# Kernel tuning notes

Measured on AMD Instinct MI355X. Metric: run time of the kernel, lower is better.

Reference implementation:

```python
import jax, jax.numpy as jnp
import numpy as np

def setup_inputs() -> dict:
    key = jax.random.key(0)
    k1, k2, k3, k4, k5 = jax.random.split(key, 5)
    H = 1024
    B, T = 32, 1024
    hidden = jax.random.normal(k1, (1, B, H), dtype=jnp.float32)
    encoder_outputs = jax.random.normal(k2, (B, T, H), dtype=jnp.float32)
    # nn.Linear(2H, H): weight [H, 2H], bias [H]
    bound = 1.0 / np.sqrt(2 * H)
    W = jax.random.uniform(k3, (H, 2 * H), minval=-bound, maxval=bound, dtype=jnp.float32)
    b = jax.random.uniform(k4, (H,), minval=-bound, maxval=bound, dtype=jnp.float32)
    v = jax.random.uniform(k5, (H,), dtype=jnp.float32)  # torch.rand
    return {"hidden": hidden, "encoder_outputs": encoder_outputs, "W": W, "b": b, "v": v}

def reference(hidden, encoder_outputs, W, b, v):
    B = hidden.shape[1]
    H = hidden.shape[2]
    h = jnp.transpose(hidden, (1, 0, 2)).reshape(B, -1)  # [B, H]
    # Split Linear(2H->H): cat([h_rep, enc]) @ W.T == h @ Wh.T + enc @ We.T
    Wh, We = W[:, :H], W[:, H:]
    # [B,1,H] + [B,T,H] -> [B,T,H]
    pre = jnp.tanh((h @ Wh.T + b)[:, None, :] + jnp.einsum('bth,gh->btg', encoder_outputs, We))
    energies = jnp.einsum('bth,h->bt', pre, v)  # [B, T]
    return jax.nn.softmax(energies, axis=1)[:, None, :]  # [B, 1, T]
```

## Files before the change

kernel.cpp:

```cpp
#include <hip/hip_runtime.h>
#include <hip/hip_fp16.h>

typedef _Float16 half8   __attribute__((ext_vector_type(8)));
typedef _Float16 half4_t __attribute__((ext_vector_type(4)));
typedef float    f32x4   __attribute__((ext_vector_type(4)));

#define HDIM  1024
#define BATCH 32
#define TLEN  1024
#define M_TOT (BATCH * TLEN)

#define BM 128
#define BN 128
#define BKF 64
#define LDA 40

__global__ void prep_k(const float* __restrict__ W, const float* __restrict__ hidden,
                       const float* __restrict__ bias, _Float16* __restrict__ We16,
                       float* __restrict__ q, float* __restrict__ energ) {
    const int bid = blockIdx.x;
    const int t = threadIdx.x;
    if (bid < 1024) {
        int idx = bid * 256 + t;
        int g  = idx >> 8;
        int k4 = idx & 255;
        float4 f = *reinterpret_cast<const float4*>(W + (size_t)g * 2048 + 1024 + k4 * 4);
        half4_t h;
        h[0] = (_Float16)f.x; h[1] = (_Float16)f.y; h[2] = (_Float16)f.z; h[3] = (_Float16)f.w;
        *reinterpret_cast<half4_t*>(We16 + (size_t)idx * 4) = h;
    } else if (bid < 2048) {
        int g = bid - 1024;
        int wave = t >> 6, lane = t & 63;
        float acc[BATCH];
#pragma unroll
        for (int b = 0; b < BATCH; b++) acc[b] = 0.f;
        const float* wr = W + (size_t)g * 2048;
        for (int h = t; h < HDIM; h += 256) {
            float w = wr[h];
#pragma unroll
            for (int b = 0; b < BATCH; b++) acc[b] = fmaf(w, hidden[b * HDIM + h], acc[b]);
        }
        __shared__ float sm[4 * BATCH];
#pragma unroll
        for (int b = 0; b < BATCH; b++) {
            float s = acc[b];
#pragma unroll
            for (int off = 32; off >= 1; off >>= 1) s += __shfl_xor(s, off);
            if (lane == 0) sm[wave * BATCH + b] = s;
        }
        __syncthreads();
        if (t < BATCH) {
            float s = sm[t] + sm[BATCH + t] + sm[2 * BATCH + t] + sm[3 * BATCH + t];
            q[t * HDIM + g] = s + bias[g];
        }
    } else {
        energ[(bid - 2048) * 256 + t] = 0.f;
    }
}

__global__ void enc_convert_k(const float* __restrict__ enc, _Float16* __restrict__ enc16) {
    size_t i = ((size_t)blockIdx.x * blockDim.x + threadIdx.x) * 8;
    float4 f0 = *reinterpret_cast<const float4*>(enc + i);
    float4 f1 = *reinterpret_cast<const float4*>(enc + i + 4);
    half8 h;
    h[0] = (_Float16)f0.x; h[1] = (_Float16)f0.y; h[2] = (_Float16)f0.z; h[3] = (_Float16)f0.w;
    h[4] = (_Float16)f1.x; h[5] = (_Float16)f1.y; h[6] = (_Float16)f1.z; h[7] = (_Float16)f1.w;
    *reinterpret_cast<half8*>(enc16 + i) = h;
}

__device__ __forceinline__ void async16(const void* g, void* l) {
    __builtin_amdgcn_global_load_lds(
        (const __attribute__((address_space(1))) void*)g,
        (__attribute__((address_space(3))) void*)l, 16, 0, 0);
}

__global__ __launch_bounds__(256)
void attn_gemm_lds_k(const _Float16* __restrict__ enc16,
                     const _Float16* __restrict__ We16,
                     const float* __restrict__ q, const float* __restrict__ v,
                     float* __restrict__ energies) {
    __shared__ _Float16 As[BM * BKF];
    __shared__ _Float16 Bs[BN * BKF];

    const int tid  = threadIdx.x;
    const int id   = blockIdx.x;
    const int xcd  = id & 7;
    const int w    = id >> 3;
    const int m0   = (xcd * 32 + (w >> 3)) * BM;
    const int n0   = (w & 7) * BN;
    const int wave = tid >> 6;
    const int lane = tid & 63;
    const int quad = lane >> 4;
    const int l16  = lane & 15;
    const int wm   = (wave & 1) * 64;
    const int wn   = (wave >> 1) * 64;

    f32x4 acc[4][4];
#pragma unroll
    for (int i = 0; i < 4; i++)
#pragma unroll
        for (int j = 0; j < 4; j++) acc[i][j] = {0.f, 0.f, 0.f, 0.f};

    const int srow = wave * 32 + (lane >> 3);
    const int scol = ((lane & 7) ^ (lane >> 3)) * 8;
    const _Float16* gA = enc16 + (size_t)(m0 + srow) * HDIM + scol;
    const _Float16* gB = We16  + (size_t)(n0 + srow) * HDIM + scol;
    _Float16* lA = As + wave * 2048;
    _Float16* lB = Bs + wave * 2048;
    const size_t istep = (size_t)8 * HDIM;

#pragma unroll
    for (int ii = 0; ii < 4; ii++) {
        async16(gA + ii * istep, lA + ii * 512);
        async16(gB + ii * istep, lB + ii * 512);
    }
    __syncthreads();

    int aoff[2][4], boff[2][4];
#pragma unroll
    for (int s = 0; s < 2; s++)
#pragma unroll
        for (int i = 0; i < 4; i++) {
            int ra = wm + i * 16 + l16;
            int rb = wn + i * 16 + l16;
            aoff[s][i] = ra * BKF + (((s * 4 + quad) ^ (l16 & 7)) * 8);
            boff[s][i] = rb * BKF + (((s * 4 + quad) ^ (l16 & 7)) * 8);
        }

    for (int k0 = 0; k0 < HDIM; k0 += BKF) {
        half8 af[2][4], bf[2][4];
#pragma unroll
        for (int s = 0; s < 2; s++)
#pragma unroll
            for (int i = 0; i < 4; i++) {
                af[s][i] = *reinterpret_cast<const half8*>(&As[aoff[s][i]]);
                bf[s][i] = *reinterpret_cast<const half8*>(&Bs[boff[s][i]]);
            }
        __syncthreads();

        if (k0 + BKF < HDIM) {
            const int kn = k0 + BKF;
#pragma unroll
            for (int ii = 0; ii < 4; ii++) {
                async16(gA + kn + ii * istep, lA + ii * 512);
                async16(gB + kn + ii * istep, lB + ii * 512);
            }
        }

#pragma unroll
        for (int s = 0; s < 2; s++)
#pragma unroll
            for (int mi = 0; mi < 4; mi++)
#pragma unroll
                for (int ni = 0; ni < 4; ni++)
                    acc[mi][ni] = __builtin_amdgcn_mfma_f32_16x16x32_f16(af[s][mi], bf[s][ni], acc[mi][ni], 0, 0, 0);

        __syncthreads();
    }

    const int bidx = m0 >> 10;
    float qv[4], vv[4];
#pragma unroll
    for (int ni = 0; ni < 4; ni++) {
        int g = n0 + wn + ni * 16 + l16;
        qv[ni] = q[bidx * HDIM + g];
        vv[ni] = v[g];
    }
#pragma unroll
    for (int mi = 0; mi < 4; mi++) {
#pragma unroll
        for (int r = 0; r < 4; r++) {
            int row = wm + mi * 16 + quad * 4 + r;
            float s = 0.f;
#pragma unroll
            for (int ni = 0; ni < 4; ni++) {
                float pre = acc[mi][ni][r] + qv[ni];
                float e = __expf(2.f * pre);
                float th = 1.f - 2.f / (e + 1.f);
                s = fmaf(th, vv[ni], s);
            }
            s += __shfl_xor(s, 1);
            s += __shfl_xor(s, 2);
            s += __shfl_xor(s, 4);
            s += __shfl_xor(s, 8);
            if (l16 == 0) atomicAdd(&energies[m0 + row], s);
        }
    }
}

__global__ __launch_bounds__(256, 2)
void attn_gemm_k(const float* __restrict__ enc, const _Float16* __restrict__ We16,
                 const float* __restrict__ q, const float* __restrict__ v,
                 float* __restrict__ energies) {
    __shared__ _Float16 As[BM * LDA];
    __shared__ _Float16 Bs[BN * LDA];

    const int tid  = threadIdx.x;
    const int m0   = blockIdx.x * BM;
    const int n0   = blockIdx.y * BN;
    const int wave = tid >> 6;
    const int lane = tid & 63;
    const int quad = lane >> 4;
    const int l16  = lane & 15;
    const int wm   = (wave & 1) * 64;
    const int wn   = (wave >> 1) * 64;

    const int srow = tid >> 1;
    const int scol = (tid & 1) * 16;

    f32x4 acc[4][4];
#pragma unroll
    for (int i = 0; i < 4; i++)
#pragma unroll
        for (int j = 0; j < 4; j++) acc[i][j] = {0.f, 0.f, 0.f, 0.f};

    const float*    ag = enc  + (size_t)(m0 + srow) * HDIM + scol;
    const _Float16* bg = We16 + (size_t)(n0 + srow) * HDIM + scol;
    _Float16* aw = &As[srow * LDA + scol];
    _Float16* bw = &Bs[srow * LDA + scol];

    for (int k0 = 0; k0 < HDIM; k0 += 32) {
        float4 a0 = *reinterpret_cast<const float4*>(ag + k0 + 0);
        float4 a1 = *reinterpret_cast<const float4*>(ag + k0 + 4);
        float4 a2 = *reinterpret_cast<const float4*>(ag + k0 + 8);
        float4 a3 = *reinterpret_cast<const float4*>(ag + k0 + 12);
        float4 b0 = *reinterpret_cast<const float4*>(bg + k0);
        float4 b1 = *reinterpret_cast<const float4*>(bg + k0 + 8);

        __syncthreads();

        half8 ha0, ha1;
        ha0[0] = (_Float16)a0.x; ha0[1] = (_Float16)a0.y; ha0[2] = (_Float16)a0.z; ha0[3] = (_Float16)a0.w;
        ha0[4] = (_Float16)a1.x; ha0[5] = (_Float16)a1.y; ha0[6] = (_Float16)a1.z; ha0[7] = (_Float16)a1.w;
        ha1[0] = (_Float16)a2.x; ha1[1] = (_Float16)a2.y; ha1[2] = (_Float16)a2.z; ha1[3] = (_Float16)a2.w;
        ha1[4] = (_Float16)a3.x; ha1[5] = (_Float16)a3.y; ha1[6] = (_Float16)a3.z; ha1[7] = (_Float16)a3.w;
        *reinterpret_cast<half8*>(aw)     = ha0;
        *reinterpret_cast<half8*>(aw + 8) = ha1;
        *reinterpret_cast<float4*>(bw)     = b0;
        *reinterpret_cast<float4*>(bw + 8) = b1;

        __syncthreads();

        half8 af[4], bf[4];
#pragma unroll
        for (int i = 0; i < 4; i++) {
            af[i] = *reinterpret_cast<const half8*>(&As[(wm + i * 16 + l16) * LDA + quad * 8]);
            bf[i] = *reinterpret_cast<const half8*>(&Bs[(wn + i * 16 + l16) * LDA + quad * 8]);
        }
#pragma unroll
        for (int mi = 0; mi < 4; mi++)
#pragma unroll
            for (int ni = 0; ni < 4; ni++)
                acc[mi][ni] = __builtin_amdgcn_mfma_f32_16x16x32_f16(af[mi], bf[ni], acc[mi][ni], 0, 0, 0);
    }

    const int bidx = m0 >> 10;
    float qv[4], vv[4];
#pragma unroll
    for (int ni = 0; ni < 4; ni++) {
        int g = n0 + wn + ni * 16 + l16;
        qv[ni] = q[bidx * HDIM + g];
        vv[ni] = v[g];
    }
#pragma unroll
    for (int mi = 0; mi < 4; mi++) {
#pragma unroll
        for (int r = 0; r < 4; r++) {
            int row = wm + mi * 16 + quad * 4 + r;
            float s = 0.f;
#pragma unroll
            for (int ni = 0; ni < 4; ni++) {
                float pre = acc[mi][ni][r] + qv[ni];
                float e = __expf(2.f * pre);
                float th = 1.f - 2.f / (e + 1.f);
                s = fmaf(th, vv[ni], s);
            }
            s += __shfl_xor(s, 1);
            s += __shfl_xor(s, 2);
            s += __shfl_xor(s, 4);
            s += __shfl_xor(s, 8);
            if (l16 == 0) atomicAdd(&energies[m0 + row], s);
        }
    }
}

__global__ void softmax_k(const float* __restrict__ energies, float* __restrict__ out) {
    int b = blockIdx.x;
    int t = threadIdx.x;
    int wave = t >> 6, lane = t & 63;
    __shared__ float smax[4], ssum[4];
    float e[4];
#pragma unroll
    for (int i = 0; i < 4; i++) e[i] = energies[b * TLEN + t + i * 256];
    float m = fmaxf(fmaxf(e[0], e[1]), fmaxf(e[2], e[3]));
#pragma unroll
    for (int off = 32; off >= 1; off >>= 1) m = fmaxf(m, __shfl_xor(m, off));
    if (lane == 0) smax[wave] = m;
    __syncthreads();
    float M = fmaxf(fmaxf(smax[0], smax[1]), fmaxf(smax[2], smax[3]));
    float x[4]; float s = 0.f;
#pragma unroll
    for (int i = 0; i < 4; i++) { x[i] = __expf(e[i] - M); s += x[i]; }
#pragma unroll
    for (int off = 32; off >= 1; off >>= 1) s += __shfl_xor(s, off);
    if (lane == 0) ssum[wave] = s;
    __syncthreads();
    float S = ssum[0] + ssum[1] + ssum[2] + ssum[3];
    float inv = 1.f / S;
#pragma unroll
    for (int i = 0; i < 4; i++) out[b * TLEN + t + i * 256] = x[i] * inv;
}

extern "C" void kernel_launch(void* const* d_in, const int* in_sizes, int n_in,
                              void* d_out, int out_size, void* d_ws, size_t ws_size,
                              hipStream_t stream) {
    const float* hidden = (const float*)d_in[0];
    const float* enc    = (const float*)d_in[1];
    const float* W      = (const float*)d_in[2];
    const float* bias   = (const float*)d_in[3];
    const float* v      = (const float*)d_in[4];
    float* out = (float*)d_out;

    char* ws = (char*)d_ws;
    float*    q     = (float*)ws;
    float*    energ = (float*)(ws + 131072);
    _Float16* We16  = (_Float16*)(ws + 262144);
    _Float16* enc16 = (_Float16*)(ws + 262144 + 2097152);
    const size_t need_fast = 262144 + 2097152 + (size_t)M_TOT * HDIM * 2;

    prep_k<<<dim3(2176), 256, 0, stream>>>(W, hidden, bias, We16, q, energ);
    if (ws_size >= need_fast) {
        enc_convert_k<<<dim3((size_t)M_TOT * HDIM / 8 / 256), 256, 0, stream>>>(enc, enc16);
        attn_gemm_lds_k<<<dim3(2048), 256, 0, stream>>>(enc16, We16, q, v, energ);
    } else {
        attn_gemm_k<<<dim3(256, 8), 256, 0, stream>>>(enc, We16, q, v, energ);
    }
    softmax_k<<<dim3(BATCH), 256, 0, stream>>>(energ, out);
}
```

Measured before the change: 317.6 us.

## Double-buffer LDS tiles with smaller K-step to overlap loads and MFMA

```diff
diff --git a/kernel.cpp b/kernel.cpp
--- a/kernel.cpp
+++ b/kernel.cpp
@@ -12,7 +12,7 @@
 
 #define BM 128
 #define BN 128
-#define BKF 64
+#define BKF 32
 #define LDA 40
 
 __global__ void prep_k(const float* __restrict__ W, const float* __restrict__ hidden,
@@ -74,13 +74,13 @@
         (__attribute__((address_space(3))) void*)l, 16, 0, 0);
 }
 
-__global__ __launch_bounds__(256)
+__global__ __launch_bounds__(256, 4)
 void attn_gemm_lds_k(const _Float16* __restrict__ enc16,
                      const _Float16* __restrict__ We16,
                      const float* __restrict__ q, const float* __restrict__ v,
                      float* __restrict__ energies) {
-    __shared__ _Float16 As[BM * BKF];
-    __shared__ _Float16 Bs[BN * BKF];
+    __shared__ _Float16 As[2][BM * BKF];
+    __shared__ _Float16 Bs[2][BN * BKF];
 
     const int tid  = threadIdx.x;
     const int id   = blockIdx.x;
@@ -101,59 +101,49 @@
 #pragma unroll
         for (int j = 0; j < 4; j++) acc[i][j] = {0.f, 0.f, 0.f, 0.f};
 
-    const int srow = wave * 32 + (lane >> 3);
-    const int scol = ((lane & 7) ^ (lane >> 3)) * 8;
-    const _Float16* gA = enc16 + (size_t)(m0 + srow) * HDIM + scol;
-    const _Float16* gB = We16  + (size_t)(n0 + srow) * HDIM + scol;
-    _Float16* lA = As + wave * 2048;
-    _Float16* lB = Bs + wave * 2048;
-    const size_t istep = (size_t)8 * HDIM;
-
-#pragma unroll
-    for (int ii = 0; ii < 4; ii++) {
-        async16(gA + ii * istep, lA + ii * 512);
-        async16(gB + ii * istep, lB + ii * 512);
-    }
+    const int srow   = wave * 32 + (lane >> 2);
+    const int fchunk = (lane & 3) ^ ((lane >> 3) & 3);
+    const _Float16* gA = enc16 + (size_t)(m0 + srow) * HDIM + fchunk * 8;
+    const _Float16* gB = We16  + (size_t)(n0 + srow) * HDIM + fchunk * 8;
+    const size_t istep = (size_t)16 * HDIM;
+    const int ldst = wave * 1024;
+
+    async16(gA, &As[0][ldst]);
+    async16(gA + istep, &As[0][ldst + 512]);
+    async16(gB, &Bs[0][ldst]);
+    async16(gB + istep, &Bs[0][ldst + 512]);
     __syncthreads();
 
-    int aoff[2][4], boff[2][4];
-#pragma unroll
-    for (int s = 0; s < 2; s++)
+    int aoff[4], boff[4];
+#pragma unroll
+    for (int i = 0; i < 4; i++) {
+        int ra = wm + i * 16 + l16;
+        int rb = wn + i * 16 + l16;
+        aoff[i] = ra * BKF + ((quad ^ ((ra >> 1) & 3)) * 8);
+        boff[i] = rb * BKF + ((quad ^ ((rb >> 1) & 3)) * 8);
+    }
+
+    for (int it = 0; it < HDIM / BKF; it++) {
+        const int p = it & 1;
+        if (it + 1 < HDIM / BKF) {
+            const int kn = (it + 1) * BKF;
+            async16(gA + kn, &As[1 - p][ldst]);
+            async16(gA + kn + istep, &As[1 - p][ldst + 512]);
+            async16(gB + kn, &Bs[1 - p][ldst]);
+            async16(gB + kn + istep, &Bs[1 - p][ldst + 512]);
+        }
+
+        half8 af[4], bf[4];
 #pragma unroll
         for (int i = 0; i < 4; i++) {
-            int ra = wm + i * 16 + l16;
-            int rb = wn + i * 16 + l16;
-            aoff[s][i] = ra * BKF + (((s * 4 + quad) ^ (l16 & 7)) * 8);
-            boff[s][i] = rb * BKF + (((s * 4 + quad) ^ (l16 & 7)) * 8);
-        }
-
-    for (int k0 = 0; k0 < HDIM; k0 += BKF) {
-        half8 af[2][4], bf[2][4];
-#pragma unroll
-        for (int s = 0; s < 2; s++)
-#pragma unroll
-            for (int i = 0; i < 4; i++) {
-                af[s][i] = *reinterpret_cast<const half8*>(&As[aoff[s][i]]);
-                bf[s][i] = *reinterpret_cast<const half8*>(&Bs[boff[s][i]]);
-            }
-        __syncthreads();
-
-        if (k0 + BKF < HDIM) {
-            const int kn = k0 + BKF;
-#pragma unroll
-            for (int ii = 0; ii < 4; ii++) {
-                async16(gA + kn + ii * istep, lA + ii * 512);
-                async16(gB + kn + ii * istep, lB + ii * 512);
-            }
-        }
-
-#pragma unroll
-        for (int s = 0; s < 2; s++)
-#pragma unroll
-            for (int mi = 0; mi < 4; mi++)
-#pragma unroll
-                for (int ni = 0; ni < 4; ni++)
-                    acc[mi][ni] = __builtin_amdgcn_mfma_f32_16x16x32_f16(af[s][mi], bf[s][ni], acc[mi][ni], 0, 0, 0);
+            af[i] = *reinterpret_cast<const half8*>(&As[p][aoff[i]]);
+            bf[i] = *reinterpret_cast<const half8*>(&Bs[p][boff[i]]);
+        }
+#pragma unroll
+        for (int mi = 0; mi < 4; mi++)
+#pragma unroll
+            for (int ni = 0; ni < 4; ni++)
+                acc[mi][ni] = __builtin_amdgcn_mfma_f32_16x16x32_f16(af[mi], bf[ni], acc[mi][ni], 0, 0, 0);
 
         __syncthreads();
     }
```

Result: slower. 327.0 us (+3.0%).

## Use 256x256 tiles with register-staged double-buffered LDS in fp16 GEMM

Applied to the files above, without the earlier changes.

```diff
diff --git a/kernel.cpp b/kernel.cpp
--- a/kernel.cpp
+++ b/kernel.cpp
@@ -10,9 +10,10 @@
 #define TLEN  1024
 #define M_TOT (BATCH * TLEN)
 
-#define BM 128
-#define BN 128
-#define BKF 64
+#define BMF 256
+#define BNF 256
+#define BKF 32
+#define NIT (HDIM / BKF)
 #define LDA 40
 
 __global__ void prep_k(const float* __restrict__ W, const float* __restrict__ hidden,
@@ -68,112 +69,137 @@
     *reinterpret_cast<half8*>(enc16 + i) = h;
 }
 
-__device__ __forceinline__ void async16(const void* g, void* l) {
-    __builtin_amdgcn_global_load_lds(
-        (const __attribute__((address_space(1))) void*)g,
-        (__attribute__((address_space(3))) void*)l, 16, 0, 0);
-}
-
-__global__ __launch_bounds__(256)
-void attn_gemm_lds_k(const _Float16* __restrict__ enc16,
+__global__ __launch_bounds__(256, 1)
+void attn_gemm_big_k(const _Float16* __restrict__ enc16,
                      const _Float16* __restrict__ We16,
                      const float* __restrict__ q, const float* __restrict__ v,
                      float* __restrict__ energies) {
-    __shared__ _Float16 As[BM * BKF];
-    __shared__ _Float16 Bs[BN * BKF];
+    __shared__ _Float16 As[2][BMF * BKF];
+    __shared__ _Float16 Bs[2][BNF * BKF];
 
     const int tid  = threadIdx.x;
     const int id   = blockIdx.x;
     const int xcd  = id & 7;
     const int w    = id >> 3;
-    const int m0   = (xcd * 32 + (w >> 3)) * BM;
-    const int n0   = (w & 7) * BN;
+    const int m0   = (xcd * 16 + (w >> 2)) * BMF;
+    const int n0   = (w & 3) * BNF;
     const int wave = tid >> 6;
     const int lane = tid & 63;
     const int quad = lane >> 4;
     const int l16  = lane & 15;
-    const int wm   = (wave & 1) * 64;
-    const int wn   = (wave >> 1) * 64;
-
-    f32x4 acc[4][4];
-#pragma unroll
-    for (int i = 0; i < 4; i++)
-#pragma unroll
-        for (int j = 0; j < 4; j++) acc[i][j] = {0.f, 0.f, 0.f, 0.f};
-
-    const int srow = wave * 32 + (lane >> 3);
-    const int scol = ((lane & 7) ^ (lane >> 3)) * 8;
-    const _Float16* gA = enc16 + (size_t)(m0 + srow) * HDIM + scol;
-    const _Float16* gB = We16  + (size_t)(n0 + srow) * HDIM + scol;
-    _Float16* lA = As + wave * 2048;
-    _Float16* lB = Bs + wave * 2048;
-    const size_t istep = (size_t)8 * HDIM;
-
-#pragma unroll
-    for (int ii = 0; ii < 4; ii++) {
-        async16(gA + ii * istep, lA + ii * 512);
-        async16(gB + ii * istep, lB + ii * 512);
+    const int wm   = (wave & 1) * 128;
+    const int wn   = (wave >> 1) * 128;
+
+    f32x4 acc[8][8];
+#pragma unroll
+    for (int i = 0; i < 8; i++)
+#pragma unroll
+        for (int j = 0; j < 8; j++) acc[i][j] = {0.f, 0.f, 0.f, 0.f};
+
+    const _Float16* gA = enc16 + (size_t)(m0 + tid) * HDIM;
+    const _Float16* gB = We16  + (size_t)(n0 + tid) * HDIM;
+    const int wsw  = (tid >> 1) & 3;
+    const int wbase = tid * BKF;
+
+    half8 rA0[4], rB0[4], rA1[4], rB1[4];
+
+#pragma unroll
+    for (int j = 0; j < 4; j++) {
+        rA0[j] = *reinterpret_cast<const half8*>(gA + j * 8);
+        rB0[j] = *reinterpret_cast<const half8*>(gB + j * 8);
+        rA1[j] = *reinterpret_cast<const half8*>(gA + BKF + j * 8);
+        rB1[j] = *reinterpret_cast<const half8*>(gB + BKF + j * 8);
+    }
+#pragma unroll
+    for (int j = 0; j < 4; j++) {
+        *reinterpret_cast<half8*>(&As[0][wbase + ((j ^ wsw) * 8)]) = rA0[j];
+        *reinterpret_cast<half8*>(&Bs[0][wbase + ((j ^ wsw) * 8)]) = rB0[j];
     }
     __syncthreads();
 
-    int aoff[2][4], boff[2][4];
-#pragma unroll
-    for (int s = 0; s < 2; s++)
-#pragma unroll
-        for (int i = 0; i < 4; i++) {
-            int ra = wm + i * 16 + l16;
-            int rb = wn + i * 16 + l16;
-            aoff[s][i] = ra * BKF + (((s * 4 + quad) ^ (l16 & 7)) * 8);
-            boff[s][i] = rb * BKF + (((s * 4 + quad) ^ (l16 & 7)) * 8);
-        }
-
-    for (int k0 = 0; k0 < HDIM; k0 += BKF) {
-        half8 af[2][4], bf[2][4];
-#pragma unroll
-        for (int s = 0; s < 2; s++)
-#pragma unroll
-            for (int i = 0; i < 4; i++) {
-                af[s][i] = *reinterpret_cast<const half8*>(&As[aoff[s][i]]);
-                bf[s][i] = *reinterpret_cast<const half8*>(&Bs[boff[s][i]]);
-            }
-        __syncthreads();
-
-        if (k0 + BKF < HDIM) {
-            const int kn = k0 + BKF;
-#pragma unroll
-            for (int ii = 0; ii < 4; ii++) {
-                async16(gA + kn + ii * istep, lA + ii * 512);
-                async16(gB + kn + ii * istep, lB + ii * 512);
-            }
-        }
-
-#pragma unroll
-        for (int s = 0; s < 2; s++)
-#pragma unroll
-            for (int mi = 0; mi < 4; mi++)
-#pragma unroll
-                for (int ni = 0; ni < 4; ni++)
-                    acc[mi][ni] = __builtin_amdgcn_mfma_f32_16x16x32_f16(af[s][mi], bf[s][ni], acc[mi][ni], 0, 0, 0);
-
+    int aoff[8], boff[8];
+#pragma unroll
+    for (int i = 0; i < 8; i++) {
+        int ra = wm + i * 16 + l16;
+        int rb = wn + i * 16 + l16;
+        aoff[i] = ra * BKF + ((quad ^ ((ra >> 1) & 3)) * 8);
+        boff[i] = rb * BKF + ((quad ^ ((rb >> 1) & 3)) * 8);
+    }
+
+    for (int it = 0; it < NIT; it += 2) {
+        if (it + 2 < NIT) {
+            const int k = (it + 2) * BKF;
+#pragma unroll
+            for (int j = 0; j < 4; j++) {
+                rA0[j] = *reinterpret_cast<const half8*>(gA + k + j * 8);
+                rB0[j] = *reinterpret_cast<const half8*>(gB + k + j * 8);
+            }
+        }
+#pragma unroll
+        for (int j = 0; j < 4; j++) {
+            *reinterpret_cast<half8*>(&As[1][wbase + ((j ^ wsw) * 8)]) = rA1[j];
+            *reinterpret_cast<half8*>(&Bs[1][wbase + ((j ^ wsw) * 8)]) = rB1[j];
+        }
+        {
+            half8 bf[8];
+#pragma unroll
+            for (int i = 0; i < 8; i++) bf[i] = *reinterpret_cast<const half8*>(&Bs[0][boff[i]]);
+#pragma unroll
+            for (int mi = 0; mi < 8; mi++) {
+                half8 af = *reinterpret_cast<const half8*>(&As[0][aoff[mi]]);
+#pragma unroll
+                for (int ni = 0; ni < 8; ni++)
+                    acc[mi][ni] = __builtin_amdgcn_mfma_f32_16x16x32_f16(af, bf[ni], acc[mi][ni], 0, 0, 0);
+            }
+        }
+        __syncthreads();
+
+        if (it + 3 < NIT) {
+            const int k = (it + 3) * BKF;
+#pragma unroll
+            for (int j = 0; j < 4; j++) {
+                rA1[j] = *reinterpret_cast<const half8*>(gA + k + j * 8);
+                rB1[j] = *reinterpret_cast<const half8*>(gB + k + j * 8);
+            }
+        }
+        if (it + 2 < NIT) {
+#pragma unroll
+            for (int j = 0; j < 4; j++) {
+                *reinterpret_cast<half8*>(&As[0][wbase + ((j ^ wsw) * 8)]) = rA0[j];
+                *reinterpret_cast<half8*>(&Bs[0][wbase + ((j ^ wsw) * 8)]) = rB0[j];
+            }
+        }
+        {
+            half8 bf[8];
+#pragma unroll
+            for (int i = 0; i < 8; i++) bf[i] = *reinterpret_cast<const half8*>(&Bs[1][boff[i]]);
+#pragma unroll
+            for (int mi = 0; mi < 8; mi++) {
+                half8 af = *reinterpret_cast<const half8*>(&As[1][aoff[mi]]);
+#pragma unroll
+                for (int ni = 0; ni < 8; ni++)
+                    acc[mi][ni] = __builtin_amdgcn_mfma_f32_16x16x32_f16(af, bf[ni], acc[mi][ni], 0, 0, 0);
+            }
+        }
         __syncthreads();
     }
 
     const int bidx = m0 >> 10;
-    float qv[4], vv[4];
-#pragma unroll
-    for (int ni = 0; ni < 4; ni++) {
+    float qv[8], vv[8];
+#pragma unroll
+    for (int ni = 0; ni < 8; ni++) {
         int g = n0 + wn + ni * 16 + l16;
         qv[ni] = q[bidx * HDIM + g];
         vv[ni] = v[g];
     }
 #pragma unroll
-    for (int mi = 0; mi < 4; mi++) {
+    for (int mi = 0; mi < 8; mi++) {
 #pragma unroll
         for (int r = 0; r < 4; r++) {
             int row = wm + mi * 16 + quad * 4 + r;
             float s = 0.f;
 #pragma unroll
-            for (int ni = 0; ni < 4; ni++) {
+            for (int ni = 0; ni < 8; ni++) {
                 float pre = acc[mi][ni][r] + qv[ni];
                 float e = __expf(2.f * pre);
                 float th = 1.f - 2.f / (e + 1.f);
@@ -192,12 +218,12 @@
 void attn_gemm_k(const float* __restrict__ enc, const _Float16* __restrict__ We16,
                  const float* __restrict__ q, const float* __restrict__ v,
                  float* __restrict__ energies) {
-    __shared__ _Float16 As[BM * LDA];
-    __shared__ _Float16 Bs[BN * LDA];
+    __shared__ _Float16 As[128 * LDA];
+    __shared__ _Float16 Bs[128 * LDA];
 
     const int tid  = threadIdx.x;
-    const int m0   = blockIdx.x * BM;
-    const int n0   = blockIdx.y * BN;
+    const int m0   = blockIdx.x * 128;
+    const int n0   = blockIdx.y * 128;
     const int wave = tid >> 6;
     const int lane = tid & 63;
     const int quad = lane >> 4;
@@ -331,7 +357,7 @@
     prep_k<<<dim3(2176), 256, 0, stream>>>(W, hidden, bias, We16, q, energ);
     if (ws_size >= need_fast) {
         enc_convert_k<<<dim3((size_t)M_TOT * HDIM / 8 / 256), 256, 0, stream>>>(enc, enc16);
-        attn_gemm_lds_k<<<dim3(2048), 256, 0, stream>>>(enc16, We16, q, v, energ);
+        attn_gemm_big_k<<<dim3(512), 256, 0, stream>>>(enc16, We16, q, v, energ);
     } else {
         attn_gemm_k<<<dim3(256, 8), 256, 0, stream>>>(enc, We16, q, v, energ);
     }
```

Result: slower. 543.1 us (+71.0%).
